# Performance work log

Hardware: AMD Instinct MI355X
Metric: run time of the kernel (lower is better)

## Reference

```python
import jax, jax.numpy as jnp
import numpy as np

S, B, D, NH, DH, L, V, DI = 1024, 4, 768, 12, 64, 4, 32000, 3072


def layer_norm(x, g, b, eps=1e-5):
    mu = jnp.mean(x, axis=-1, keepdims=True)
    var = jnp.mean((x - mu) ** 2, axis=-1, keepdims=True)
    return (x - mu) * jax.lax.rsqrt(var + eps) * g + b


def sinusoid_pos_emb():
    # PositionalEmbedding: ger(pos_seq, inv_freq) then [sin, cos]
    pos_seq = jnp.arange(S - 1, -1, -1, dtype=jnp.float32)
    inv_freq = 1.0 / (10000.0 ** (jnp.arange(0.0, D, 2.0) / D))
    si = pos_seq[:, None] * inv_freq[None, :]
    return jnp.concatenate([jnp.sin(si), jnp.cos(si)], axis=-1)  # (S, D)


def setup_inputs() -> dict:
    key = jax.random.key(0)
    ks = jax.random.split(key, 16)
    w = 0.02
    inp = jax.random.randint(ks[0], (S, B), 0, V)
    word_emb = jax.random.normal(ks[1], (V, D)) * w
    Wq = jax.random.normal(ks[2], (L, D, D)) * w
    Wkv = jax.random.normal(ks[3], (L, 2 * D, D)) * w
    Wo = jax.random.normal(ks[4], (L, D, D)) * w
    ln1_g = jnp.ones((L, D)); ln1_b = jnp.zeros((L, D))
    ffW1 = jax.random.normal(ks[5], (L, DI, D)) * w
    ffb1 = jnp.zeros((L, DI))
    ffW2 = jax.random.normal(ks[6], (L, D, DI)) * w
    ffb2 = jnp.zeros((L, D))
    ln2_g = jnp.ones((L, D)); ln2_b = jnp.zeros((L, D))
    # pre-populated InfiniAttn memory state; norm kept strictly positive
    memory = jax.random.normal(ks[7], (L, B, NH, DH, DH)) * jnp.sqrt(jnp.float32(S))
    mem_norm = jax.random.uniform(ks[8], (L, B, NH, DH)) * S + 0.5 * S
    return dict(inp=inp, word_emb=word_emb, Wq=Wq, Wkv=Wkv, Wo=Wo,
                ln1_g=ln1_g, ln1_b=ln1_b, ffW1=ffW1, ffb1=ffb1,
                ffW2=ffW2, ffb2=ffb2, ln2_g=ln2_g, ln2_b=ln2_b,
                memory=memory, mem_norm=mem_norm)


def reference(inp, word_emb, Wq, Wkv, Wo, ln1_g, ln1_b, ffW1, ffb1, ffW2, ffb2,
              ln2_g, ln2_b, memory, mem_norm):
    emb_scale = D ** 0.5
    h = word_emb[inp] * emb_scale + sinusoid_pos_emb()[:, None, :]  # (S,B,D)
    causal = jnp.triu(jnp.ones((S, S), dtype=bool), k=1)  # mask j > i
    scale = 1.0 / DH ** 0.5
    gate = jax.nn.sigmoid(jnp.float32(0.01))  # sigmoid(beta), beta_eps=0.01 (buffer)
    neg_inf = jnp.finfo(h.dtype).min
    new_mems, new_norms = [], []
    for l in range(L):
        q = (h @ Wq[l].T).reshape(S, B, NH, DH)
        kv = h @ Wkv[l].T
        k, v = jnp.split(kv, 2, axis=-1)
        k = k.reshape(S, B, NH, DH)
        v = v.reshape(S, B, NH, DH)
        score = jnp.einsum('ibnd,jbnd->ijbn', q, k) * scale
        score = jnp.where(causal[:, :, None, None], neg_inf, score)
        prob = jax.nn.softmax(score, axis=1)
        attn_vec = jnp.einsum('ijbn,jbnd->ibnd', prob, v).reshape(S, B, NH * DH)
        # NOTE: original calls _update_memory(head_q, head_v, head_k), i.e. K=v, V=k
        Qb = jnp.swapaxes(q, 0, 1)  # (B,S,n,d)
        Kb = jnp.swapaxes(v, 0, 1)
        Vb = jnp.swapaxes(k, 0, 1)
        cQ = jax.nn.elu(Qb) + 1.0
        cK = jax.nn.elu(Kb) + 1.0
        # memory retrieval (detached in the original)
        num = jnp.einsum('bsnk,bnkv->bsnv', cQ, memory[l])
        den = jnp.einsum('bsnk,bnk->bsn', cQ, mem_norm[l])[..., None]
        content_A = jax.lax.stop_gradient(num / den)  # (B,S,n,d)
        # memory update with delta trick (no_grad in the original)
        numK = jnp.einsum('bsnk,bnkv->bsnv', cK, memory[l])
        denK = jnp.einsum('bsnk,bnk->bsn', cK, mem_norm[l])[..., None]
        delta = numK / denK
        new_mems.append(jax.lax.stop_gradient(
            memory[l] + jnp.einsum('bsnk,bsnv->bnkv', cK, Vb - delta)))
        new_norms.append(jax.lax.stop_gradient(mem_norm[l] + cK.sum(axis=1)))
        # gated injection of memory content into local attention output
        attn_vec = gate * jnp.swapaxes(content_A, 0, 1).reshape(S, B, NH * DH) \
                   + (1.0 - gate) * attn_vec
        out = layer_norm(h + attn_vec @ Wo[l].T, ln1_g[l], ln1_b[l])
        core = jax.nn.relu(out @ ffW1[l].T + ffb1[l]) @ ffW2[l].T + ffb2[l]
        h = layer_norm(out + core, ln2_g[l], ln2_b[l])
    return h, jnp.stack(new_mems), jnp.stack(new_norms)
```

## Files before the change

### kernel.cpp

```cpp
#include <hip/hip_runtime.h>
#include <hip/hip_bf16.h>
#include <math.h>

#define S 1024
#define B 4
#define Dm 768
#define NH 12
#define DH 64
#define NL 4
#define DI 3072
#define QS 2304
#define MU_CHUNK 8
#define NROW (S * B * NH)

typedef __hip_bfloat16 bf16;
typedef short bf16x8 __attribute__((ext_vector_type(8)));
typedef float f32x4 __attribute__((ext_vector_type(4)));

__device__ __forceinline__ float b2f(bf16 x) { return __bfloat162float(x); }
__device__ __forceinline__ bf16 f2b(float x) { return __float2bfloat16(x); }

__device__ __forceinline__ float ldv(const float* p, size_t i) { return p[i]; }
__device__ __forceinline__ float ldv(const bf16* p, size_t i) { return b2f(p[i]); }

__device__ __forceinline__ float wave_sum(float x) {
  #pragma unroll
  for (int off = 32; off > 0; off >>= 1) x += __shfl_xor(x, off, 64);
  return x;
}

typedef const __attribute__((address_space(1))) unsigned int guint;
typedef __attribute__((address_space(3))) unsigned int luint;
__device__ __forceinline__ void async_cp16(const void* g, void* l) {
  __builtin_amdgcn_global_load_lds((guint*)g, (luint*)l, 16, 0, 0);
}

__global__ void embed_kernel(const int* __restrict__ inp, const float* __restrict__ wemb,
                             float* __restrict__ h, bf16* __restrict__ hb) {
  int idx = blockIdx.x * blockDim.x + threadIdx.x;
  if (idx >= S * B * Dm) return;
  int d = idx % Dm;
  int sb = idx / Dm;
  int b = sb % B;
  int s = sb / B;
  int tok = inp[s * B + b];
  float e = wemb[(size_t)tok * Dm + d] * 27.712812921102035f;
  float ps = (float)(S - 1 - s);
  float pe;
  if (d < Dm / 2) {
    float invf = expf(-(2.0f * (float)d / (float)Dm) * 9.210340371976184f);
    pe = sinf(ps * invf);
  } else {
    int j = d - Dm / 2;
    float invf = expf(-(2.0f * (float)j / (float)Dm) * 9.210340371976184f);
    pe = cosf(ps * invf);
  }
  float val = e + pe;
  h[idx] = val;
  hb[idx] = f2b(val);
}

#define SEG_QKV 1769472
#define SEG_WO  2359296
#define SEG_W1  4718592
#define SEG_END 7077888
__global__ void convw_kernel(const float* __restrict__ Wq, const float* __restrict__ Wkv,
                             const float* __restrict__ Wo, const float* __restrict__ W1,
                             const float* __restrict__ W2, bf16* __restrict__ dst) {
  int idx = (blockIdx.x * blockDim.x + threadIdx.x) * 4;
  if (idx >= SEG_END) return;
  const float* src;
  if (idx < SEG_QKV) {
    src = (idx < 589824) ? Wq + idx : Wkv + (idx - 589824);
  } else if (idx < SEG_WO) {
    src = Wo + (idx - SEG_QKV);
  } else if (idx < SEG_W1) {
    src = W1 + (idx - SEG_WO);
  } else {
    src = W2 + (idx - SEG_W1);
  }
  float4 f = *(const float4*)src;
  bf16 b0 = f2b(f.x), b1 = f2b(f.y), b2 = f2b(f.z), b3 = f2b(f.w);
  unsigned short o[4];
  o[0] = *(unsigned short*)&b0; o[1] = *(unsigned short*)&b1;
  o[2] = *(unsigned short*)&b2; o[3] = *(unsigned short*)&b3;
  *(uint2*)((unsigned short*)dst + idx) = *(uint2*)o;
}

template <int MREP, int RELU, int SPLITK, typename OT>
__global__ __launch_bounds__(256) void gemm_async(const bf16* __restrict__ A,
                                                  const bf16* __restrict__ W,
                                                  const float* __restrict__ bias,
                                                  OT* __restrict__ C,
                                                  int ldc, int K) {
  constexpr int BM = MREP * 32;
  __shared__ __align__(16) unsigned short Asm[2][BM * 32];
  __shared__ __align__(16) unsigned short Bsm[2][128 * 32];
  const int t = threadIdx.x;
  const int w = t >> 6, lane = t & 63;
  const int col = lane & 15, quad = lane >> 4;
  const int wm = w >> 1, wn = w & 1;
  const int m0 = blockIdx.y * BM, n0 = blockIdx.x * 128;
  const int Kc = K / SPLITK;
  const int kbeg = (SPLITK > 1) ? blockIdx.z * Kc : 0;

  const bf16* aSrc = A + (size_t)(m0 + w * 16 + col) * K + kbeg + quad * 8;
  const bf16* bSrc = W + (size_t)(n0 + w * 16 + col) * K + kbeg + quad * 8;

  const f32x4 zf = {0.0f, 0.0f, 0.0f, 0.0f};
  f32x4 acc[MREP][4];
  #pragma unroll
  for (int mt = 0; mt < MREP; mt++)
    #pragma unroll
    for (int nt = 0; nt < 4; nt++) acc[mt][nt] = zf;

  #pragma unroll
  for (int i = 0; i < MREP / 2; i++)
    async_cp16(aSrc + (size_t)i * 64 * K, &Asm[0][i * 2048 + w * 512]);
  #pragma unroll
  for (int i = 0; i < 2; i++)
    async_cp16(bSrc + (size_t)i * 64 * K, &Bsm[0][i * 2048 + w * 512]);
  __syncthreads();

  int cur = 0;
  for (int kk = 32; kk < Kc; kk += 32) {
    #pragma unroll
    for (int i = 0; i < MREP / 2; i++)
      async_cp16(aSrc + kk + (size_t)i * 64 * K, &Asm[cur ^ 1][i * 2048 + w * 512]);
    #pragma unroll
    for (int i = 0; i < 2; i++)
      async_cp16(bSrc + kk + (size_t)i * 64 * K, &Bsm[cur ^ 1][i * 2048 + w * 512]);
    bf16x8 af[MREP], bfr[4];
    #pragma unroll
    for (int mt = 0; mt < MREP; mt++)
      af[mt] = *(const bf16x8*)&Asm[cur][(wm * MREP + mt) * 512 + lane * 8];
    #pragma unroll
    for (int nt = 0; nt < 4; nt++)
      bfr[nt] = *(const bf16x8*)&Bsm[cur][(wn * 4 + nt) * 512 + lane * 8];
    #pragma unroll
    for (int mt = 0; mt < MREP; mt++)
      #pragma unroll
      for (int nt = 0; nt < 4; nt++)
        acc[mt][nt] = __builtin_amdgcn_mfma_f32_16x16x32_bf16(af[mt], bfr[nt],
                                                              acc[mt][nt], 0, 0, 0);
    __syncthreads();
    cur ^= 1;
  }
  {
    bf16x8 af[MREP], bfr[4];
    #pragma unroll
    for (int mt = 0; mt < MREP; mt++)
      af[mt] = *(const bf16x8*)&Asm[cur][(wm * MREP + mt) * 512 + lane * 8];
    #pragma unroll
    for (int nt = 0; nt < 4; nt++)
      bfr[nt] = *(const bf16x8*)&Bsm[cur][(wn * 4 + nt) * 512 + lane * 8];
    #pragma unroll
    for (int mt = 0; mt < MREP; mt++)
      #pragma unroll
      for (int nt = 0; nt < 4; nt++)
        acc[mt][nt] = __builtin_amdgcn_mfma_f32_16x16x32_bf16(af[mt], bfr[nt],
                                                              acc[mt][nt], 0, 0, 0);
  }

  OT* Cb = C;
  if (SPLITK > 1)
    Cb = C + (size_t)blockIdx.z * gridDim.y * BM * ldc;
  #pragma unroll
  for (int nt = 0; nt < 4; nt++) {
    const int colg = n0 + wn * 64 + nt * 16 + col;
    const float bv = bias ? bias[colg] : 0.0f;
    #pragma unroll
    for (int mt = 0; mt < MREP; mt++) {
      #pragma unroll
      for (int r = 0; r < 4; r++) {
        const int row = m0 + wm * (MREP * 16) + mt * 16 + quad * 4 + r;
        float val = acc[mt][nt][r] + bv;
        if (RELU) val = fmaxf(val, 0.0f);
        if constexpr (__is_same(OT, float)) {
          Cb[(size_t)row * ldc + colg] = val;
        } else {
          Cb[(size_t)row * ldc + colg] = f2b(val);
        }
      }
    }
  }
}

template <int NSLICE, int RELU>
__global__ void gemmred_kernel(const float* __restrict__ part, const float* __restrict__ bias,
                               bf16* __restrict__ out, int N, size_t MN) {
  size_t i4 = ((size_t)blockIdx.x * blockDim.x + threadIdx.x) * 4;
  if (i4 >= MN) return;
  float4 a = *(const float4*)(part + i4);
  #pragma unroll
  for (int z = 1; z < NSLICE; z++) {
    float4 p = *(const float4*)(part + (size_t)z * MN + i4);
    a.x += p.x; a.y += p.y; a.z += p.z; a.w += p.w;
  }
  if (bias) {
    int colb = (int)(i4 % N);
    a.x += bias[colb]; a.y += bias[colb + 1]; a.z += bias[colb + 2]; a.w += bias[colb + 3];
  }
  if (RELU) {
    a.x = fmaxf(a.x, 0.0f); a.y = fmaxf(a.y, 0.0f);
    a.z = fmaxf(a.z, 0.0f); a.w = fmaxf(a.w, 0.0f);
  }
  bf16 b0 = f2b(a.x), b1 = f2b(a.y), b2 = f2b(a.z), b3 = f2b(a.w);
  unsigned short o[4];
  o[0] = *(unsigned short*)&b0; o[1] = *(unsigned short*)&b1;
  o[2] = *(unsigned short*)&b2; o[3] = *(unsigned short*)&b3;
  *(uint2*)((unsigned short*)out + i4) = *(uint2*)o;
}

template <int SPLIT>
__global__ __launch_bounds__(256) void attn_flash(const bf16* __restrict__ q,
                                                  const bf16* __restrict__ k,
                                                  const bf16* __restrict__ v,
                                                  bf16* __restrict__ att,
                                                  bf16* __restrict__ po0,
                                                  bf16* __restrict__ po1,
                                                  float* __restrict__ pml) {
  const int it = blockIdx.x;
  const int bn = blockIdx.y;
  const int b = bn / NH, n = bn % NH;
  const int t = threadIdx.x;
  const int w = t >> 6, lane = t & 63;
  const int col = lane & 15, quad = lane >> 4;
  const int i0 = it * 64;

  int jbeg = 0, jend = it + 1;
  if (SPLIT == 2) {
    const int half = (it + 2) >> 1;
    if (blockIdx.z == 0) jend = half; else jbeg = half;
    if (jbeg >= jend) return;
  }

  __shared__ __align__(16) unsigned short Kt[64 * 72];
  __shared__ __align__(16) unsigned short Vt[64 * 72];
  __shared__ __align__(16) unsigned short Pw[64 * 72];

  const unsigned short* qp = (const unsigned short*)q;
  const unsigned short* kp = (const unsigned short*)k;
  const unsigned short* vp = (const unsigned short*)v;

  bf16x8 aq[2];
  {
    size_t qb = ((size_t)(i0 + w * 16 + col) * B + b) * QS + n * DH + quad * 8;
    aq[0] = *(const bf16x8*)(qp + qb);
    aq[1] = *(const bf16x8*)(qp + qb + 32);
  }

  const f32x4 zf = {0.0f, 0.0f, 0.0f, 0.0f};
  float mrow[4], lrow[4];
  f32x4 o[4];
  #pragma unroll
  for (int r = 0; r < 4; r++) { mrow[r] = -1e30f; lrow[r] = 0.0f; }
  #pragma unroll
  for (int db = 0; db < 4; db++) o[db] = zf;

  const int jj = t >> 2;
  const int d0 = (t & 3) << 4;

  uint4 rk0, rk1, rv0, rv1;
  {
    size_t gb = ((size_t)(jbeg * 64 + jj) * B + b) * QS + n * DH + d0;
    rk0 = *(const uint4*)(kp + gb); rk1 = *(const uint4*)(kp + gb + 8);
    rv0 = *(const uint4*)(vp + gb); rv1 = *(const uint4*)(vp + gb + 8);
  }

  for (int jt = jbeg; jt < jend; jt++) {
    const int j0 = jt * 64;
    __syncthreads();
    {
      *(uint4*)&Kt[jj * 72 + d0] = rk0;
      *(uint4*)&Kt[jj * 72 + d0 + 8] = rk1;
      unsigned short tv[16];
      *(uint4*)tv = rv0;
      *(uint4*)(tv + 8) = rv1;
      #pragma unroll
      for (int x = 0; x < 16; x++) Vt[(d0 + x) * 72 + jj] = tv[x];
    }
    __syncthreads();
    if (jt + 1 < jend) {
      size_t gb = ((size_t)((jt + 1) * 64 + jj) * B + b) * QS + n * DH + d0;
      rk0 = *(const uint4*)(kp + gb); rk1 = *(const uint4*)(kp + gb + 8);
      rv0 = *(const uint4*)(vp + gb); rv1 = *(const uint4*)(vp + gb + 8);
    }

    f32x4 sf[4];
    #pragma unroll
    for (int nb = 0; nb < 4; nb++) sf[nb] = zf;
    #pragma unroll
    for (int ks = 0; ks < 2; ks++) {
      #pragma unroll
      for (int nb = 0; nb < 4; nb++) {
        bf16x8 kb = *(const bf16x8*)&Kt[(nb * 16 + col) * 72 + ks * 32 + quad * 8];
        sf[nb] = __builtin_amdgcn_mfma_f32_16x16x32_bf16(aq[ks], kb, sf[nb], 0, 0, 0);
      }
    }

    const bool diag = (jt == it);
    #pragma unroll
    for (int r = 0; r < 4; r++) {
      const int irow = i0 + w * 16 + quad * 4 + r;
      float sv[4];
      #pragma unroll
      for (int nb = 0; nb < 4; nb++) {
        float s = sf[nb][r] * 0.125f;
        if (diag && (j0 + nb * 16 + col) > irow) s = -1e30f;
        sv[nb] = s;
      }
      float rm = fmaxf(fmaxf(sv[0], sv[1]), fmaxf(sv[2], sv[3]));
      #pragma unroll
      for (int off = 8; off > 0; off >>= 1) rm = fmaxf(rm, __shfl_xor(rm, off, 64));
      const float mn = fmaxf(mrow[r], rm);
      const float alpha = __expf(mrow[r] - mn);
      mrow[r] = mn;
      float ps = 0.0f;
      #pragma unroll
      for (int nb = 0; nb < 4; nb++) {
        float p = __expf(sv[nb] - mn);
        ps += p;
        bf16 hb = f2b(p);
        Pw[(w * 16 + quad * 4 + r) * 72 + nb * 16 + col] = *(unsigned short*)&hb;
      }
      #pragma unroll
      for (int off = 8; off > 0; off >>= 1) ps += __shfl_xor(ps, off, 64);
      lrow[r] = lrow[r] * alpha + ps;
      #pragma unroll
      for (int db = 0; db < 4; db++) o[db][r] *= alpha;
    }

    #pragma unroll
    for (int ks = 0; ks < 2; ks++) {
      bf16x8 pa = *(const bf16x8*)&Pw[(w * 16 + col) * 72 + ks * 32 + quad * 8];
      #pragma unroll
      for (int db = 0; db < 4; db++) {
        bf16x8 vb = *(const bf16x8*)&Vt[(db * 16 + col) * 72 + ks * 32 + quad * 8];
        o[db] = __builtin_amdgcn_mfma_f32_16x16x32_bf16(pa, vb, o[db], 0, 0, 0);
      }
    }
  }

  if (SPLIT == 1) {
    unsigned short* ap = (unsigned short*)att;
    #pragma unroll
    for (int r = 0; r < 4; r++) {
      const int irow = i0 + w * 16 + quad * 4 + r;
      const float inv = 1.0f / lrow[r];
      size_t ob = ((size_t)irow * B + b) * Dm + n * DH + col;
      #pragma unroll
      for (int db = 0; db < 4; db++) {
        bf16 hb = f2b(o[db][r] * inv);
        ap[ob + db * 16] = *(unsigned short*)&hb;
      }
    }
  } else {
    unsigned short* pp = (unsigned short*)(blockIdx.z ? po1 : po0);
    float* pm = pml + (size_t)blockIdx.z * 2 * NROW;
    float* pl = pm + NROW;
    #pragma unroll
    for (int r = 0; r < 4; r++) {
      const int irow = i0 + w * 16 + quad * 4 + r;
      const float inv = 1.0f / lrow[r];
      size_t ob = ((size_t)irow * B + b) * Dm + n * DH + col;
      #pragma unroll
      for (int db = 0; db < 4; db++) {
        bf16 hb = f2b(o[db][r] * inv);
        pp[ob + db * 16] = *(unsigned short*)&hb;
      }
      if (col == 0) {
        int rix = (irow * B + b) * NH + n;
        pm[rix] = mrow[r];
        pl[rix] = lrow[r];
      }
    }
  }
}

__global__ void attn_comb(const bf16* __restrict__ po0, const bf16* __restrict__ po1,
                          const float* __restrict__ pml, bf16* __restrict__ att) {
  size_t i4 = ((size_t)blockIdx.x * blockDim.x + threadIdx.x) * 4;
  if (i4 >= (size_t)S * B * Dm) return;
  int sb = (int)(i4 / Dm);
  int dd = (int)(i4 % Dm);
  int srow = sb / B;
  int it = srow >> 6;
  uint2 a0 = *(const uint2*)((const unsigned short*)po0 + i4);
  if (it == 0) {
    *(uint2*)((unsigned short*)att + i4) = a0;
    return;
  }
  uint2 a1 = *(const uint2*)((const unsigned short*)po1 + i4);
  int rix = sb * NH + (dd >> 6);
  float m0 = pml[rix],            l0 = pml[NROW + rix];
  float m1 = pml[2 * NROW + rix], l1 = pml[3 * NROW + rix];
  float M = fmaxf(m0, m1);
  float w0 = l0 * __expf(m0 - M), w1 = l1 * __expf(m1 - M);
  float inv = 1.0f / (w0 + w1);
  const unsigned short* p0 = (const unsigned short*)&a0;
  const unsigned short* p1 = (const unsigned short*)&a1;
  unsigned short o[4];
  #pragma unroll
  for (int j = 0; j < 4; j++) {
    float val = (w0 * b2f(*(const bf16*)&p0[j]) + w1 * b2f(*(const bf16*)&p1[j])) * inv;
    bf16 hb = f2b(val);
    o[j] = *(unsigned short*)&hb;
  }
  *(uint2*)((unsigned short*)att + i4) = *(uint2*)o;
}

__global__ __launch_bounds__(256) void meminfer_mfma(const bf16* __restrict__ qkv,
                                                     const float* __restrict__ mem,
                                                     const float* __restrict__ mnorm,
                                                     bf16* __restrict__ att,
                                                     bf16* __restrict__ vd) {
  const int s0 = blockIdx.x * 64;
  const int bn = blockIdx.y;
  const int b = bn / NH, n = bn % NH;
  const int t = threadIdx.x;
  const int w = t >> 6, lane = t & 63;
  const int col = lane & 15, quad = lane >> 4;

  __shared__ __align__(16) unsigned short CQ[4096];
  __shared__ __align__(16) unsigned short CK[4096];
  __shared__ __align__(16) unsigned short Bm[5120];

  const unsigned short* qp = (const unsigned short*)qkv;

  {
    int r = t >> 2;
    int k0 = (t & 3) * 16;
    size_t gb = ((size_t)(s0 + r) * B + b) * QS + n * DH + k0;
    int abase = (r >> 4) * 1024 + (k0 >> 5) * 512 + ((k0 & 31) >> 3) * 128 + (r & 15) * 8;
    unsigned short tq[16], tv[16], oq[16], ov[16];
    *(uint4*)tq = *(const uint4*)(qp + gb);
    *(uint4*)(tq + 8) = *(const uint4*)(qp + gb + 8);
    *(uint4*)tv = *(const uint4*)(qp + gb + 1536);
    *(uint4*)(tv + 8) = *(const uint4*)(qp + gb + 1536 + 8);
    #pragma unroll
    for (int i = 0; i < 16; i++) {
      float fq = b2f(*(const bf16*)&tq[i]);
      float fv = b2f(*(const bf16*)&tv[i]);
      float eq = fq > 0.0f ? fq + 1.0f : __expf(fq);
      float ev = fv > 0.0f ? fv + 1.0f : __expf(fv);
      bf16 bq = f2b(eq), bv2 = f2b(ev);
      oq[i] = *(unsigned short*)&bq;
      ov[i] = *(unsigned short*)&bv2;
    }
    *(bf16x8*)&CQ[abase] = *(bf16x8*)oq;
    *(bf16x8*)&CQ[abase + 128] = *(bf16x8*)(oq + 8);
    *(bf16x8*)&CK[abase] = *(bf16x8*)ov;
    *(bf16x8*)&CK[abase + 128] = *(bf16x8*)(ov + 8);
  }
  {
    int v = t & 63, kb = (t >> 6) * 16;
    const float* mp = mem + (size_t)bn * DH * DH;
    #pragma unroll
    for (int i = 0; i < 16; i++) {
      int k = kb + i;
      bf16 mb = f2b(mp[(size_t)k * DH + v]);
      int addr = (v >> 4) * 1024 + (k >> 5) * 512 + ((k & 31) >> 3) * 128 + (v & 15) * 8 + (k & 7);
      Bm[addr] = *(unsigned short*)&mb;
    }
  }
  {
    int a = t * 4;
    int m = (a >> 3) & 15;
    int kk = (a >> 9) * 32 + ((a >> 7) & 3) * 8 + (a & 7);
    unsigned short vals[4] = {0, 0, 0, 0};
    if (m == 0) {
      const float* np = mnorm + (size_t)bn * DH;
      #pragma unroll
      for (int j = 0; j < 4; j++) {
        bf16 nb = f2b(np[kk + j]);
        vals[j] = *(unsigned short*)&nb;
      }
    }
    *(uint2*)&Bm[4096 + a] = *(uint2*)vals;
  }
  __syncthreads();

  const f32x4 zf = {0.0f, 0.0f, 0.0f, 0.0f};
  f32x4 aq[5], ak[5];
  #pragma unroll
  for (int nb = 0; nb < 5; nb++) { aq[nb] = zf; ak[nb] = zf; }
  #pragma unroll
  for (int ks = 0; ks < 2; ks++) {
    bf16x8 fq = *(const bf16x8*)&CQ[w * 1024 + ks * 512 + lane * 8];
    bf16x8 fk = *(const bf16x8*)&CK[w * 1024 + ks * 512 + lane * 8];
    #pragma unroll
    for (int nb = 0; nb < 5; nb++) {
      bf16x8 bm = *(const bf16x8*)&Bm[nb * 1024 + ks * 512 + lane * 8];
      aq[nb] = __builtin_amdgcn_mfma_f32_16x16x32_bf16(fq, bm, aq[nb], 0, 0, 0);
      ak[nb] = __builtin_amdgcn_mfma_f32_16x16x32_bf16(fk, bm, ak[nb], 0, 0, 0);
    }
  }

  const float gate = 1.0f / (1.0f + expf(-0.01f));
  unsigned short* ap = (unsigned short*)att;
  unsigned short* vp2 = (unsigned short*)vd;
  #pragma unroll
  for (int r = 0; r < 4; r++) {
    const int srow = s0 + w * 16 + quad * 4 + r;
    const float denq = __shfl(aq[4][r], lane & 48, 64);
    const float denk = __shfl(ak[4][r], lane & 48, 64);
    const size_t bd = ((size_t)srow * B + b) * Dm + n * DH + col;
    const size_t bq = ((size_t)srow * B + b) * QS + 768 + n * DH + col;
    #pragma unroll
    for (int nb = 0; nb < 4; nb++) {
      float content = aq[nb][r] / denq;
      float delta = ak[nb][r] / denk;
      float attv = b2f(*(const bf16*)&ap[bd + nb * 16]);
      bf16 ao = f2b(gate * content + (1.0f - gate) * attv);
      ap[bd + nb * 16] = *(unsigned short*)&ao;
      float kvv = b2f(*(const bf16*)&qp[bq + nb * 16]);
      bf16 vo = f2b(kvv - delta);
      vp2[bd + nb * 16] = *(unsigned short*)&vo;
    }
  }
}

__global__ void memupd_kernel(const bf16* __restrict__ qkv, const bf16* __restrict__ vd,
                              float* __restrict__ part, float* __restrict__ pnorm) {
  int bn = blockIdx.x % (B * NH);
  int c = blockIdx.x / (B * NH);
  int b = bn / NH, n = bn % NH;
  int t = threadIdx.x;
  int k = t >> 2;
  int v0 = (t & 3) * 16;
  __shared__ float ckl[8][DH];
  __shared__ float vdl[8][DH];
  float acc[16];
  #pragma unroll
  for (int j = 0; j < 16; j++) acc[j] = 0.0f;
  float nsum = 0.0f;
  const int sBeg = c * (S / MU_CHUNK), sEnd = sBeg + S / MU_CHUNK;
  for (int s0 = sBeg; s0 < sEnd; s0 += 8) {
    #pragma unroll
    for (int i2 = 0; i2 < 2; i2++) {
      int idx = t + i2 * 256;
      int sp = idx >> 6, dd = idx & 63;
      int gq = ((s0 + sp) * B + b) * QS + 1536 + n * DH + dd;
      int gd = ((s0 + sp) * B + b) * Dm + n * DH + dd;
      float vv = b2f(qkv[gq]);
      ckl[sp][dd] = vv > 0.0f ? vv + 1.0f : expf(vv);
      vdl[sp][dd] = b2f(vd[gd]);
    }
    __syncthreads();
    #pragma unroll
    for (int sp = 0; sp < 8; sp++) {
      float cc = ckl[sp][k];
      if ((t & 3) == 0) nsum += cc;
      #pragma unroll
      for (int j = 0; j < 16; j++) acc[j] += cc * vdl[sp][v0 + j];
    }
    __syncthreads();
  }
  float* prow = part + (size_t)c * (B * NH * DH * DH) + (size_t)bn * DH * DH;
  #pragma unroll
  for (int j4 = 0; j4 < 4; j4++) {
    float4 o;
    o.x = acc[j4 * 4 + 0]; o.y = acc[j4 * 4 + 1];
    o.z = acc[j4 * 4 + 2]; o.w = acc[j4 * 4 + 3];
    *(float4*)&prow[k * DH + v0 + j4 * 4] = o;
  }
  if ((t & 3) == 0) pnorm[(size_t)c * (B * NH * DH) + bn * DH + k] = nsum;
}

__global__ void memred_kernel(const float* __restrict__ mem, const float* __restrict__ mnorm,
                              const float* __restrict__ part, const float* __restrict__ pnorm,
                              float* __restrict__ out_mem, float* __restrict__ out_norm) {
  const int MEMN = B * NH * DH * DH;
  int i = blockIdx.x * blockDim.x + threadIdx.x;
  if (i < MEMN / 4) {
    int i4 = i * 4;
    float4 a = *(const float4*)(mem + i4);
    #pragma unroll
    for (int c = 0; c < MU_CHUNK; c++) {
      float4 p = *(const float4*)(part + (size_t)c * MEMN + i4);
      a.x += p.x; a.y += p.y; a.z += p.z; a.w += p.w;
    }
    *(float4*)(out_mem + i4) = a;
  } else {
    int j4 = (i - MEMN / 4) * 4;
    if (j4 < B * NH * DH) {
      float4 a = *(const float4*)(mnorm + j4);
      #pragma unroll
      for (int c = 0; c < MU_CHUNK; c++) {
        float4 p = *(const float4*)(pnorm + (size_t)c * (B * NH * DH) + j4);
        a.x += p.x; a.y += p.y; a.z += p.z; a.w += p.w;
      }
      *(float4*)(out_norm + j4) = a;
    }
  }
}

template <typename TX, typename TY>
__global__ void addln_kernel(const TX* __restrict__ x, const TY* __restrict__ y,
                             const float* __restrict__ g, const float* __restrict__ bb,
                             float* __restrict__ outf, bf16* __restrict__ outb) {
  int row = blockIdx.x;
  int t = threadIdx.x;
  float vals[3];
  float sum = 0.0f, sq = 0.0f;
  #pragma unroll
  for (int i = 0; i < 3; i++) {
    size_t idx = (size_t)row * Dm + t + i * 256;
    float vv = ldv(x, idx) + ldv(y, idx);
    vals[i] = vv;
    sum += vv;
    sq += vv * vv;
  }
  sum = wave_sum(sum);
  sq = wave_sum(sq);
  __shared__ float s1[4], s2[4];
  int w = t >> 6, lane = t & 63;
  if (lane == 0) { s1[w] = sum; s2[w] = sq; }
  __syncthreads();
  if (t == 0) {
    s1[0] = s1[0] + s1[1] + s1[2] + s1[3];
    s2[0] = s2[0] + s2[1] + s2[2] + s2[3];
  }
  __syncthreads();
  sum = s1[0]; sq = s2[0];
  float mu = sum / 768.0f;
  float var = sq / 768.0f - mu * mu;
  float rs = rsqrtf(var + 1e-5f);
  #pragma unroll
  for (int i = 0; i < 3; i++) {
    int d = t + i * 256;
    float o = (vals[i] - mu) * rs * g[d] + bb[d];
    size_t idx = (size_t)row * Dm + d;
    if (outf) outf[idx] = o;
    if (outb) outb[idx] = f2b(o);
  }
}

extern "C" void kernel_launch(void* const* d_in, const int* in_sizes, int n_in,
                              void* d_out, int out_size, void* d_ws, size_t ws_size,
                              hipStream_t stream) {
  (void)in_sizes; (void)n_in; (void)out_size;
  const int*   inp   = (const int*)d_in[0];
  const float* wemb  = (const float*)d_in[1];
  const float* Wq    = (const float*)d_in[2];
  const float* Wkv   = (const float*)d_in[3];
  const float* Wo    = (const float*)d_in[4];
  const float* ln1g  = (const float*)d_in[5];
  const float* ln1b  = (const float*)d_in[6];
  const float* fW1   = (const float*)d_in[7];
  const float* fb1   = (const float*)d_in[8];
  const float* fW2   = (const float*)d_in[9];
  const float* fb2   = (const float*)d_in[10];
  const float* ln2g  = (const float*)d_in[11];
  const float* ln2b  = (const float*)d_in[12];
  const float* mem   = (const float*)d_in[13];
  const float* mnorm = (const float*)d_in[14];

  const size_t SBD = (size_t)S * B * Dm;

  bf16* ws   = (bf16*)d_ws;
  bf16* qkv  = ws;
  bf16* vd   = ws + 3 * SBD;
  bf16* att  = ws + 4 * SBD;
  bf16* hbf  = att;
  bf16* ff2o = att;
  bf16* out1 = ws + 5 * SBD;
  bf16* wb   = ws + 6 * SBD;
  bf16* ffm  = ws;
  bf16* tmp  = ws;
  float* part  = (float*)out1;
  float* pnorm = (float*)(wb + SEG_END);
  float* partg = pnorm + (size_t)MU_CHUNK * B * NH * DH;
  const size_t need = ((size_t)(6 * SBD + SEG_END)) * 2 +
                      ((size_t)MU_CHUNK * B * NH * DH + 2 * SBD) * 4;
  const bool use_splitk = (ws_size >= need);
  bf16* po0 = vd;
  bf16* po1 = out1;
  float* pml = partg;

  float* h    = (float*)d_out;
  float* outm = h + SBD;
  float* outn = outm + (size_t)NL * B * NH * DH * DH;

  dim3 b256(256);
  embed_kernel<<<dim3((S * B * Dm + 255) / 256), b256, 0, stream>>>(inp, wemb, h, hbf);

  for (int l = 0; l < NL; l++) {
    convw_kernel<<<dim3(SEG_END / 4 / 256), b256, 0, stream>>>(
        Wq + (size_t)l * Dm * Dm, Wkv + (size_t)l * 2 * Dm * Dm,
        Wo + (size_t)l * Dm * Dm, fW1 + (size_t)l * DI * Dm,
        fW2 + (size_t)l * Dm * DI, wb);
    const bf16* wqkv = wb;
    const bf16* wo_b = wb + SEG_QKV;
    const bf16* w1_b = wb + SEG_WO;
    const bf16* w2_b = wb + SEG_W1;
    const float* mem_l = mem + (size_t)l * B * NH * DH * DH;
    const float* mn_l  = mnorm + (size_t)l * B * NH * DH;
    float* outm_l = outm + (size_t)l * B * NH * DH * DH;
    float* outn_l = outn + (size_t)l * B * NH * DH;

    gemm_async<4, 0, 1, bf16><<<dim3(QS / 128, 32), b256, 0, stream>>>(
        hbf, wqkv, nullptr, qkv, QS, Dm);

    if (use_splitk) {
      attn_flash<2><<<dim3(S / 64, B * NH, 2), b256, 0, stream>>>(
          qkv, qkv + 768, qkv + 1536, att, po0, po1, pml);
      attn_comb<<<dim3((unsigned)(SBD / 4 / 256)), b256, 0, stream>>>(po0, po1, pml, att);
    } else {
      attn_flash<1><<<dim3(S / 64, B * NH), b256, 0, stream>>>(
          qkv, qkv + 768, qkv + 1536, att, nullptr, nullptr, nullptr);
    }
    meminfer_mfma<<<dim3(S / 64, B * NH), b256, 0, stream>>>(qkv, mem_l, mn_l, att, vd);
    memupd_kernel<<<dim3(B * NH * MU_CHUNK), b256, 0, stream>>>(qkv, vd, part, pnorm);
    memred_kernel<<<dim3(771), b256, 0, stream>>>(mem_l, mn_l, part, pnorm, outm_l, outn_l);

    if (use_splitk) {
      gemm_async<2, 0, 2, float><<<dim3(Dm / 128, 64, 2), b256, 0, stream>>>(
          att, wo_b, nullptr, partg, Dm, Dm);
      gemmred_kernel<2, 0><<<dim3((unsigned)(SBD / 4 / 256)), b256, 0, stream>>>(
          partg, nullptr, tmp, Dm, SBD);
    } else {
      gemm_async<2, 0, 1, bf16><<<dim3(Dm / 128, 64), b256, 0, stream>>>(
          att, wo_b, nullptr, tmp, Dm, Dm);
    }
    addln_kernel<float, bf16><<<dim3(S * B), b256, 0, stream>>>(
        h, tmp, ln1g + l * Dm, ln1b + l * Dm, nullptr, out1);

    gemm_async<4, 1, 1, bf16><<<dim3(DI / 128, 32), b256, 0, stream>>>(
        out1, w1_b, fb1 + (size_t)l * DI, ffm, DI, Dm);
    if (use_splitk) {
      gemm_async<2, 0, 2, float><<<dim3(Dm / 128, 64, 2), b256, 0, stream>>>(
          ffm, w2_b, nullptr, partg, Dm, DI);
      gemmred_kernel<2, 0><<<dim3((unsigned)(SBD / 4 / 256)), b256, 0, stream>>>(
          partg, fb2 + (size_t)l * Dm, ff2o, Dm, SBD);
    } else {
      gemm_async<2, 0, 1, bf16><<<dim3(Dm / 128, 64), b256, 0, stream>>>(
          ffm, w2_b, fb2 + (size_t)l * Dm, ff2o, Dm, DI);
    }
    addln_kernel<bf16, bf16><<<dim3(S * B), b256, 0, stream>>>(
        out1, ff2o, ln2g + l * Dm, ln2b + l * Dm, h, hbf);
  }
}
```

Measured before the change: 1.338 ms.

## Fuse split-K reduction into add+LayerNorm and swizzle GEMM workgroup order

Removes the separate split-K reduction kernel and folds the sum of partial slices, plus bias, into the residual add+LayerNorm kernel, which saves one launch and a bf16 round trip per projection. The Wo and FFN2 GEMMs change from 2-way split-K with 64-row tiles to 3-way split-K with 128-row tiles. Workgroup IDs are also remapped in groups of 8, likely to match XCD placement and improve L2 locality. The third fp32 partial slice raises the workspace requirement, and if the workspace is too small the code falls back to the path without split-K.

After: 1.285 ms. 4.0% less time.

```diff
diff --git a/kernel.cpp b/kernel.cpp
--- a/kernel.cpp
+++ b/kernel.cpp
@@ -100,7 +100,19 @@
   const int w = t >> 6, lane = t & 63;
   const int col = lane & 15, quad = lane >> 4;
   const int wm = w >> 1, wn = w & 1;
-  const int m0 = blockIdx.y * BM, n0 = blockIdx.x * 128;
+
+  int bx = blockIdx.x, by = blockIdx.y;
+  {
+    const int nwg = gridDim.x * gridDim.y;
+    if ((nwg & 7) == 0) {
+      int orig = by * gridDim.x + bx;
+      int cpx = nwg >> 3;
+      int wg2 = (orig & 7) * cpx + (orig >> 3);
+      bx = wg2 % gridDim.x;
+      by = wg2 / gridDim.x;
+    }
+  }
+  const int m0 = by * BM, n0 = bx * 128;
   const int Kc = K / SPLITK;
   const int kbeg = (SPLITK > 1) ? blockIdx.z * Kc : 0;
 
@@ -184,32 +196,6 @@
       }
     }
   }
-}
-
-template <int NSLICE, int RELU>
-__global__ void gemmred_kernel(const float* __restrict__ part, const float* __restrict__ bias,
-                               bf16* __restrict__ out, int N, size_t MN) {
-  size_t i4 = ((size_t)blockIdx.x * blockDim.x + threadIdx.x) * 4;
-  if (i4 >= MN) return;
-  float4 a = *(const float4*)(part + i4);
-  #pragma unroll
-  for (int z = 1; z < NSLICE; z++) {
-    float4 p = *(const float4*)(part + (size_t)z * MN + i4);
-    a.x += p.x; a.y += p.y; a.z += p.z; a.w += p.w;
-  }
-  if (bias) {
-    int colb = (int)(i4 % N);
-    a.x += bias[colb]; a.y += bias[colb + 1]; a.z += bias[colb + 2]; a.w += bias[colb + 3];
-  }
-  if (RELU) {
-    a.x = fmaxf(a.x, 0.0f); a.y = fmaxf(a.y, 0.0f);
-    a.z = fmaxf(a.z, 0.0f); a.w = fmaxf(a.w, 0.0f);
-  }
-  bf16 b0 = f2b(a.x), b1 = f2b(a.y), b2 = f2b(a.z), b3 = f2b(a.w);
-  unsigned short o[4];
-  o[0] = *(unsigned short*)&b0; o[1] = *(unsigned short*)&b1;
-  o[2] = *(unsigned short*)&b2; o[3] = *(unsigned short*)&b3;
-  *(uint2*)((unsigned short*)out + i4) = *(uint2*)o;
 }
 
 template <int SPLIT>
@@ -608,6 +594,54 @@
   for (int i = 0; i < 3; i++) {
     size_t idx = (size_t)row * Dm + t + i * 256;
     float vv = ldv(x, idx) + ldv(y, idx);
+    vals[i] = vv;
+    sum += vv;
+    sq += vv * vv;
+  }
+  sum = wave_sum(sum);
+  sq = wave_sum(sq);
+  __shared__ float s1[4], s2[4];
+  int w = t >> 6, lane = t & 63;
+  if (lane == 0) { s1[w] = sum; s2[w] = sq; }
+  __syncthreads();
+  if (t == 0) {
+    s1[0] = s1[0] + s1[1] + s1[2] + s1[3];
+    s2[0] = s2[0] + s2[1] + s2[2] + s2[3];
+  }
+  __syncthreads();
+  sum = s1[0]; sq = s2[0];
+  float mu = sum / 768.0f;
+  float var = sq / 768.0f - mu * mu;
+  float rs = rsqrtf(var + 1e-5f);
+  #pragma unroll
+  for (int i = 0; i < 3; i++) {
+    int d = t + i * 256;
+    float o = (vals[i] - mu) * rs * g[d] + bb[d];
+    size_t idx = (size_t)row * Dm + d;
+    if (outf) outf[idx] = o;
+    if (outb) outb[idx] = f2b(o);
+  }
+}
+
+template <int NSLICE, typename TX>
+__global__ void addln_red_kernel(const TX* __restrict__ x, const float* __restrict__ part,
+                                 const float* __restrict__ bias,
+                                 const float* __restrict__ g, const float* __restrict__ bb,
+                                 float* __restrict__ outf, bf16* __restrict__ outb) {
+  const size_t SBDc = (size_t)S * B * Dm;
+  int row = blockIdx.x;
+  int t = threadIdx.x;
+  float vals[3];
+  float sum = 0.0f, sq = 0.0f;
+  #pragma unroll
+  for (int i = 0; i < 3; i++) {
+    int d = t + i * 256;
+    size_t idx = (size_t)row * Dm + d;
+    float y = part[idx];
+    #pragma unroll
+    for (int z = 1; z < NSLICE; z++) y += part[(size_t)z * SBDc + idx];
+    if (bias) y += bias[d];
+    float vv = ldv(x, idx) + y;
     vals[i] = vv;
     sum += vv;
     sq += vv * vv;
@@ -664,16 +698,16 @@
   bf16* vd   = ws + 3 * SBD;
   bf16* att  = ws + 4 * SBD;
   bf16* hbf  = att;
-  bf16* ff2o = att;
   bf16* out1 = ws + 5 * SBD;
   bf16* wb   = ws + 6 * SBD;
   bf16* ffm  = ws;
   bf16* tmp  = ws;
+  bf16* ff2o = att;
   float* part  = (float*)out1;
   float* pnorm = (float*)(wb + SEG_END);
   float* partg = pnorm + (size_t)MU_CHUNK * B * NH * DH;
   const size_t need = ((size_t)(6 * SBD + SEG_END)) * 2 +
-                      ((size_t)MU_CHUNK * B * NH * DH + 2 * SBD) * 4;
+                      ((size_t)MU_CHUNK * B * NH * DH + 3 * SBD) * 4;
   const bool use_splitk = (ws_size >= need);
   bf16* po0 = vd;
   bf16* po1 = out1;
@@ -716,29 +750,29 @@
     memred_kernel<<<dim3(771), b256, 0, stream>>>(mem_l, mn_l, part, pnorm, outm_l, outn_l);
 
     if (use_splitk) {
-      gemm_async<2, 0, 2, float><<<dim3(Dm / 128, 64, 2), b256, 0, stream>>>(
+      gemm_async<4, 0, 3, float><<<dim3(Dm / 128, 32, 3), b256, 0, stream>>>(
           att, wo_b, nullptr, partg, Dm, Dm);
-      gemmred_kernel<2, 0><<<dim3((unsigned)(SBD / 4 / 256)), b256, 0, stream>>>(
-          partg, nullptr, tmp, Dm, SBD);
+      addln_red_kernel<3, float><<<dim3(S * B), b256, 0, stream>>>(
+          h, partg, nullptr, ln1g + l * Dm, ln1b + l * Dm, nullptr, out1);
     } else {
       gemm_async<2, 0, 1, bf16><<<dim3(Dm / 128, 64), b256, 0, stream>>>(
           att, wo_b, nullptr, tmp, Dm, Dm);
-    }
-    addln_kernel<float, bf16><<<dim3(S * B), b256, 0, stream>>>(
-        h, tmp, ln1g + l * Dm, ln1b + l * Dm, nullptr, out1);
+      addln_kernel<float, bf16><<<dim3(S * B), b256, 0, stream>>>(
+          h, tmp, ln1g + l * Dm, ln1b + l * Dm, nullptr, out1);
+    }
 
     gemm_async<4, 1, 1, bf16><<<dim3(DI / 128, 32), b256, 0, stream>>>(
         out1, w1_b, fb1 + (size_t)l * DI, ffm, DI, Dm);
     if (use_splitk) {
-      gemm_async<2, 0, 2, float><<<dim3(Dm / 128, 64, 2), b256, 0, stream>>>(
+      gemm_async<4, 0, 3, float><<<dim3(Dm / 128, 32, 3), b256, 0, stream>>>(
           ffm, w2_b, nullptr, partg, Dm, DI);
-      gemmred_kernel<2, 0><<<dim3((unsigned)(SBD / 4 / 256)), b256, 0, stream>>>(
-          partg, fb2 + (size_t)l * Dm, ff2o, Dm, SBD);
+      addln_red_kernel<3, bf16><<<dim3(S * B), b256, 0, stream>>>(
+          out1, partg, fb2 + (size_t)l * Dm, ln2g + l * Dm, ln2b + l * Dm, h, hbf);
     } else {
       gemm_async<2, 0, 1, bf16><<<dim3(Dm / 128, 64), b256, 0, stream>>>(
           ffm, w2_b, fb2 + (size_t)l * Dm, ff2o, Dm, DI);
-    }
-    addln_kernel<bf16, bf16><<<dim3(S * B), b256, 0, stream>>>(
-        out1, ff2o, ln2g + l * Dm, ln2b + l * Dm, h, hbf);
-  }
-}
+      addln_kernel<bf16, bf16><<<dim3(S * B), b256, 0, stream>>>(
+          out1, ff2o, ln2g + l * Dm, ln2b + l * Dm, h, hbf);
+    }
+  }
+}
```
